# Optimization experiments

Measured on AMD Instinct MI355X. Metric: run time of the kernel, lower is better.

The kernel has to match this reference:

```python
import jax, jax.numpy as jnp
import numpy as np

D_MODEL = 1024
NUM_HEADS = 16
HEAD_DIM = D_MODEL // NUM_HEADS
FF_HIDDEN = 2 * D_MODEL
EPS = 1e-5


def _layernorm(x, g, b):
    mu = jnp.mean(x, axis=-1, keepdims=True)
    var = jnp.var(x, axis=-1, keepdims=True)
    return (x - mu) * jax.lax.rsqrt(var + EPS) * g + b


def setup_inputs() -> dict:
    key = jax.random.key(0)
    ks = jax.random.split(key, 12)
    s = lambda fan_in: 1.0 / np.sqrt(fan_in)
    return {
        "x": jax.random.normal(ks[0], (4, 2048, D_MODEL), dtype=jnp.float32),
        "qkv_w": jax.random.uniform(ks[1], (D_MODEL, 3 * D_MODEL), minval=-s(D_MODEL), maxval=s(D_MODEL)),
        "qkv_b": jax.random.uniform(ks[2], (3 * D_MODEL,), minval=-s(D_MODEL), maxval=s(D_MODEL)),
        "out_w": jax.random.uniform(ks[3], (D_MODEL, D_MODEL), minval=-s(D_MODEL), maxval=s(D_MODEL)),
        "out_b": jax.random.uniform(ks[4], (D_MODEL,), minval=-s(D_MODEL), maxval=s(D_MODEL)),
        "ff1_w": jax.random.uniform(ks[5], (D_MODEL, FF_HIDDEN), minval=-s(D_MODEL), maxval=s(D_MODEL)),
        "ff1_b": jax.random.uniform(ks[6], (FF_HIDDEN,), minval=-s(D_MODEL), maxval=s(D_MODEL)),
        "ff2_w": jax.random.uniform(ks[7], (FF_HIDDEN, D_MODEL), minval=-s(FF_HIDDEN), maxval=s(FF_HIDDEN)),
        "ff2_b": jax.random.uniform(ks[8], (D_MODEL,), minval=-s(FF_HIDDEN), maxval=s(FF_HIDDEN)),
        "ln1_g": jnp.ones((D_MODEL,), jnp.float32),
        "ln1_b": jnp.zeros((D_MODEL,), jnp.float32),
        "ln2_g": jnp.ones((D_MODEL,), jnp.float32),
        "ln2_b": jnp.zeros((D_MODEL,), jnp.float32),
    }


def reference(x, qkv_w, qkv_b, out_w, out_b, ff1_w, ff1_b, ff2_w, ff2_b, ln1_g, ln1_b, ln2_g, ln2_b):
    B, L, _ = x.shape
    scale = HEAD_DIM ** -0.5
    # pre-norm attention
    h = _layernorm(x, ln1_g, ln1_b)
    qkv = h @ qkv_w + qkv_b  # [B,L,3D]
    q, k, v = jnp.split(qkv, 3, axis=-1)
    reshape = lambda t: t.reshape(B, L, NUM_HEADS, HEAD_DIM).transpose(0, 2, 1, 3)  # [B,H,L,Dh]
    q, k, v = reshape(q), reshape(k), reshape(v)
    attn = jnp.einsum('bhqd,bhkd->bhqk', q, k) * scale  # [B,H,L,L]
    attn = jax.nn.softmax(attn, axis=-1)
    ctx = jnp.einsum('bhqk,bhkd->bhqd', attn, v)
    ctx = ctx.transpose(0, 2, 1, 3).reshape(B, L, D_MODEL)
    attended = ctx @ out_w + out_b
    x = x + attended
    # pre-norm FFN with exact GELU (torch default)
    h2 = _layernorm(x, ln2_g, ln2_b)
    ff = jax.nn.gelu(h2 @ ff1_w + ff1_b, approximate=False) @ ff2_w + ff2_b
    return x + ff
```

## Files before the change

kernel.cpp:

```cpp
#include <hip/hip_runtime.h>

#define AS1 __attribute__((address_space(1)))
#define AS3 __attribute__((address_space(3)))

typedef unsigned short u16;
typedef __bf16 bf16x8 __attribute__((ext_vector_type(8)));
typedef float floatx4 __attribute__((ext_vector_type(4)));
typedef float floatx16 __attribute__((ext_vector_type(16)));
typedef u16 u16x8 __attribute__((ext_vector_type(8)));
typedef u16 u16x4 __attribute__((ext_vector_type(4)));
typedef unsigned uintx4 __attribute__((ext_vector_type(4)));

__device__ __forceinline__ float bf2f(u16 u) { return __uint_as_float(((unsigned)u) << 16); }
__device__ __forceinline__ u16 f2bf(float f) {
    unsigned u = __float_as_uint(f);
    u += 0x7FFFu + ((u >> 16) & 1u);
    return (u16)(u >> 16);
}
__device__ __forceinline__ unsigned packbf2(float f0, float f1) {
    return __builtin_amdgcn_perm(__float_as_uint(f1), __float_as_uint(f0), 0x07060302u);
}
__device__ __forceinline__ float fexp2(float x) {
#if __has_builtin(__builtin_amdgcn_exp2f)
    return __builtin_amdgcn_exp2f(x);
#else
    float r;
    asm("v_exp_f32 %0, %1" : "=v"(r) : "v"(x));
    return r;
#endif
}
__device__ __forceinline__ void gl_lds16(const u16* g, u16* l) {
    __builtin_amdgcn_global_load_lds((const AS1 void*)g, (AS3 void*)l, 16, 0, 0);
}

__global__ __launch_bounds__(256) void transpose_all(const float* __restrict__ w0, u16* __restrict__ o0,
                                                     const float* __restrict__ w1, u16* __restrict__ o1,
                                                     const float* __restrict__ w2, u16* __restrict__ o2,
                                                     const float* __restrict__ w3, u16* __restrict__ o3) {
    __shared__ u16 t[32][33];
    int blk = blockIdx.x;
    const float* in;
    u16* out;
    int R, C, bx, by;
    if (blk < 3072) {
        in = w0; out = o0; R = 1024; C = 3072; bx = blk % 96; by = blk / 96;
    } else if (blk < 4096) {
        blk -= 3072; in = w1; out = o1; R = 1024; C = 1024; bx = blk % 32; by = blk / 32;
    } else if (blk < 6144) {
        blk -= 4096; in = w2; out = o2; R = 1024; C = 2048; bx = blk % 64; by = blk / 64;
    } else {
        blk -= 6144; in = w3; out = o3; R = 2048; C = 1024; bx = blk % 32; by = blk / 32;
    }
    const int c0 = bx * 32, r0 = by * 32;
    const int tx = threadIdx.x, ty = threadIdx.y;
#pragma unroll
    for (int i = 0; i < 4; i++)
        t[ty + i * 8][tx] = f2bf(in[(size_t)(r0 + ty + i * 8) * C + c0 + tx]);
    __syncthreads();
#pragma unroll
    for (int i = 0; i < 4; i++) out[(size_t)(c0 + ty + i * 8) * R + r0 + tx] = t[tx][ty + i * 8];
}

__global__ __launch_bounds__(256) void ln_k(const float* __restrict__ x, const float* __restrict__ g,
                                            const float* __restrict__ b, u16* __restrict__ out) {
    const int row = blockIdx.x, tid = threadIdx.x;
    const float4 xv = *(const float4*)(x + (size_t)row * 1024 + tid * 4);
    float f[4] = {xv.x, xv.y, xv.z, xv.w};
    float s1 = 0.f, s2 = 0.f;
#pragma unroll
    for (int e = 0; e < 4; e++) {
        s1 += f[e];
        s2 += f[e] * f[e];
    }
#pragma unroll
    for (int off = 32; off >= 1; off >>= 1) {
        s1 += __shfl_down(s1, off);
        s2 += __shfl_down(s2, off);
    }
    __shared__ float w1[4], w2[4];
    const int wave = tid >> 6, lane = tid & 63;
    if (lane == 0) { w1[wave] = s1; w2[wave] = s2; }
    __syncthreads();
    s1 = w1[0] + w1[1] + w1[2] + w1[3];
    s2 = w2[0] + w2[1] + w2[2] + w2[3];
    const float mu = s1 * (1.0f / 1024.0f);
    const float var = s2 * (1.0f / 1024.0f) - mu * mu;
    const float rs = rsqrtf(var + 1e-5f);
    const float4 gv = *(const float4*)(g + tid * 4);
    const float4 bv = *(const float4*)(b + tid * 4);
    const float gf[4] = {gv.x, gv.y, gv.z, gv.w}, bff[4] = {bv.x, bv.y, bv.z, bv.w};
    u16x4 o;
#pragma unroll
    for (int e = 0; e < 4; e++) o[e] = f2bf((f[e] - mu) * rs * gf[e] + bff[e]);
    *(u16x4*)(out + (size_t)row * 1024 + tid * 4) = o;
}

template <int GELU, int RESID, int F32OUT, int KSWZ>
__global__ __launch_bounds__(256, 4) void gemm_bt(const u16* __restrict__ A, const u16* __restrict__ Bt,
                                                  const float* __restrict__ bias,
                                                  const float* __restrict__ resid, void* __restrict__ Cv,
                                                  int M, int N, int K, int lda) {
    __shared__ u16 Al[2][128 * 32];
    __shared__ u16 Bl[2][128 * 32];
    const int tid = threadIdx.x;
    const int wave = tid >> 6, lane = tid & 63;
    const int g16 = lane >> 4, l16 = lane & 15;
    const int m0 = blockIdx.y * 128, n0 = blockIdx.x * 128;
    const int wm = (wave >> 1) * 64, wn = (wave & 1) * 64;
    const int csw = (l16 >> 1) & 3;

    floatx4 acc[4][4] = {};

    const int scs = ((lane & 3) ^ ((lane >> 3) & 3)) * 8;
    const u16* Ag = A + (size_t)(m0 + (lane >> 2)) * lda + scs;
    const u16* Bg = Bt + (size_t)(n0 + (lane >> 2)) * K + scs;

    auto stage = [&](int buf, int k0) {
#pragma unroll
        for (int i = 0; i < 2; i++) {
            const int ro = 16 * (wave * 2 + i);
            gl_lds16(Ag + (size_t)ro * lda + k0, &Al[buf][(wave * 2 + i) * 512]);
            gl_lds16(Bg + (size_t)ro * K + k0, &Bl[buf][(wave * 2 + i) * 512]);
        }
    };

    stage(0, 0);
    __syncthreads();
    int buf = 0;
    for (int k0 = 0; k0 < K; k0 += 32) {
        if (k0 + 32 < K) stage(buf ^ 1, k0 + 32);
        bf16x8 af[4], bfr[4];
#pragma unroll
        for (int i = 0; i < 4; i++)
            af[i] = *(const bf16x8*)&Al[buf][(wm + i * 16 + l16) * 32 + ((g16 ^ csw) << 3)];
#pragma unroll
        for (int j = 0; j < 4; j++)
            bfr[j] = *(const bf16x8*)&Bl[buf][(wn + j * 16 + l16) * 32 + ((g16 ^ csw) << 3)];
#pragma unroll
        for (int i = 0; i < 4; i++)
#pragma unroll
            for (int j = 0; j < 4; j++)
                acc[i][j] = __builtin_amdgcn_mfma_f32_16x16x32_bf16(af[i], bfr[j], acc[i][j], 0, 0, 0);
        __syncthreads();
        buf ^= 1;
    }

    float bv[4];
#pragma unroll
    for (int j = 0; j < 4; j++) bv[j] = bias[n0 + wn + j * 16 + l16];
#pragma unroll
    for (int i = 0; i < 4; i++) {
#pragma unroll
        for (int r = 0; r < 4; r++) {
            const int gm = m0 + wm + i * 16 + g16 * 4 + r;
            const size_t ro = (size_t)gm * N;
#pragma unroll
            for (int j = 0; j < 4; j++) {
                int gn = n0 + wn + j * 16 + l16;
                float v = acc[i][j][r] + bv[j];
                if (GELU) v = 0.5f * v * (1.0f + erff(v * 0.70710678118654752f));
                if (RESID) v += resid[ro + gn];
                if (KSWZ && ((gn >> 10) == 1)) gn ^= (gm & 7) << 3;
                if (F32OUT)
                    ((float*)Cv)[ro + gn] = v;
                else
                    ((u16*)Cv)[ro + gn] = f2bf(v);
            }
        }
    }
}

__global__ __launch_bounds__(256) void attn_prep(const u16* __restrict__ qkv, u16* __restrict__ Vsw) {
    __shared__ u16 Tl[64][72];
    const int bh = blockIdx.y, b = bh >> 4, h = bh & 15;
    const int kt = blockIdx.x * 64;
    const int t = threadIdx.x;
    const size_t qbase = (size_t)b * 2048 * 3072;
    const int r = t >> 2, cpi = (t & 3) * 2;

    const u16* vrow = qkv + qbase + (size_t)(kt + r) * 3072 + 2048 + h * 64;
    *(u16x8*)&Tl[r][cpi * 8] = *(const u16x8*)(vrow + cpi * 8);
    *(u16x8*)&Tl[r][(cpi + 1) * 8] = *(const u16x8*)(vrow + (cpi + 1) * 8);
    __syncthreads();
    {
        const int d = r;
        u16* dst = Vsw + ((size_t)bh * 64 + d) * 2048 + kt;
#pragma unroll
        for (int i = 0; i < 2; i++) {
            const int cp = cpi + i;
            const int c = cp ^ (d & 7);
            u16x8 tmp;
#pragma unroll
            for (int e = 0; e < 8; e++) tmp[e] = Tl[c * 8 + e][d];
            *(u16x8*)(dst + cp * 8) = tmp;
        }
    }
}

__global__ __launch_bounds__(256, 4) void attn_k(u16* __restrict__ qkv, const u16* __restrict__ Vsw) {
    __shared__ u16 Kl[2][64 * 64];
    __shared__ u16 Vt[2][64 * 64];
    const int tid = threadIdx.x;
    const int w = tid >> 6, lane = tid & 63;
    const int l31 = lane & 31, half = lane >> 5, swz = lane & 7;
    const int bh = blockIdx.y, b = bh >> 4, h = bh & 15;
    const int q0 = blockIdx.x * 128 + w * 32;
    const size_t qbase = (size_t)b * 2048 * 3072;
    const size_t vbase = (size_t)bh * 64 * 2048;

    bf16x8 bq[4];
    {
        const u16* qp = qkv + qbase + (size_t)(q0 + l31) * 3072 + h * 64;
        const float sc = 0.125f * 1.44269504088896340736f;
#pragma unroll
        for (int kd = 0; kd < 4; kd++) {
            const u16x8 raw = *(const u16x8*)(qp + kd * 16 + half * 8);
            u16 tmp[8];
#pragma unroll
            for (int e = 0; e < 8; e++) tmp[e] = f2bf(bf2f(raw[e]) * sc);
            bq[kd] = *(const bf16x8*)tmp;
        }
    }

    floatx16 accO[2] = {};
    float lsp[4] = {0.f, 0.f, 0.f, 0.f};

    auto stage = [&](int buf, int kt) {
#pragma unroll
        for (int i = 0; i < 2; i++) {
            const int rr = w * 16 + i * 8 + (lane >> 3);
            gl_lds16(qkv + qbase + (size_t)(kt + rr) * 3072 + 1024 + h * 64 + (lane & 7) * 8,
                     &Kl[buf][(w * 16 + i * 8) * 64]);
            gl_lds16(Vsw + vbase + (size_t)rr * 2048 + kt + (lane & 7) * 8,
                     &Vt[buf][(w * 16 + i * 8) * 64]);
        }
    };

    auto qk = [&](int bufi, floatx16* S) {
        floatx16 t[2] = {};
#pragma unroll
        for (int kb = 0; kb < 2; kb++)
#pragma unroll
            for (int kd = 0; kd < 4; kd++) {
                const bf16x8 ak =
                    *(const bf16x8*)&Kl[bufi][(kb * 32 + l31) * 64 + ((kd * 2 + half) ^ swz) * 8];
                t[kb] = __builtin_amdgcn_mfma_f32_32x32x16_bf16(ak, bq[kd], t[kb], 0, 0, 0);
            }
        S[0] = t[0];
        S[1] = t[1];
    };

    auto fused_sm_pv = [&](int bufi, const floatx16* S) {
#pragma unroll
        for (int kb = 0; kb < 2; kb++)
#pragma unroll
            for (int kp = 0; kp < 2; kp++) {
                float E[8];
#pragma unroll
                for (int j = 0; j < 8; j++) {
                    E[j] = fexp2(S[kb][8 * kp + j]);
                    lsp[j & 3] += E[j];
                }
                unsigned x0 = packbf2(E[0], E[1]);
                unsigned x1 = packbf2(E[2], E[3]);
                unsigned y0 = packbf2(E[4], E[5]);
                unsigned y1 = packbf2(E[6], E[7]);
                asm volatile("v_permlane32_swap_b32 %0, %1" : "+v"(x0), "+v"(y0));
                asm volatile("v_permlane32_swap_b32 %0, %1" : "+v"(x1), "+v"(y1));
                uintx4 f;
                f[0] = x0; f[1] = x1; f[2] = y0; f[3] = y1;
                const bf16x8 bp = __builtin_bit_cast(bf16x8, f);
                const int kd = kb * 2 + kp;
#pragma unroll
                for (int db = 0; db < 2; db++) {
                    const bf16x8 av =
                        *(const bf16x8*)&Vt[bufi][(db * 32 + l31) * 64 + ((kd * 2 + half) ^ swz) * 8];
                    accO[db] = __builtin_amdgcn_mfma_f32_32x32x16_bf16(av, bp, accO[db], 0, 0, 0);
                }
            }
    };

    stage(0, 0);
    __syncthreads();
    stage(1, 64);
    floatx16 accS[2];
    qk(0, accS);

    int buf = 0;
    for (int kt = 0; kt < 2048 - 64; kt += 64) {
        fused_sm_pv(buf, accS);
        __syncthreads();
        if (kt + 128 < 2048) stage(buf, kt + 128);
        __builtin_amdgcn_s_setprio(1);
        qk(buf ^ 1, accS);
        __builtin_amdgcn_s_setprio(0);
        buf ^= 1;
    }
    fused_sm_pv(buf, accS);

    float lsum = (lsp[0] + lsp[1]) + (lsp[2] + lsp[3]);
    lsum += __shfl_xor(lsum, 32);
    const float rinv = 1.0f / lsum;
    u16* cw = qkv + qbase + (size_t)(q0 + l31) * 3072 + 2048 + h * 64;
#pragma unroll
    for (int db = 0; db < 2; db++)
#pragma unroll
        for (int rg = 0; rg < 4; rg++) {
            const int d0 = db * 32 + 8 * rg + 4 * half;
            u16x4 o;
#pragma unroll
            for (int rr2 = 0; rr2 < 4; rr2++) o[rr2] = f2bf(accO[db][rg * 4 + rr2] * rinv);
            *(u16x4*)(cw + d0) = o;
        }
}

extern "C" void kernel_launch(void* const* d_in, const int* in_sizes, int n_in, void* d_out,
                              int out_size, void* d_ws, size_t ws_size, hipStream_t stream) {
    const float* x = (const float*)d_in[0];
    const float* qkv_w = (const float*)d_in[1];
    const float* qkv_b = (const float*)d_in[2];
    const float* out_w = (const float*)d_in[3];
    const float* out_b = (const float*)d_in[4];
    const float* ff1_w = (const float*)d_in[5];
    const float* ff1_b = (const float*)d_in[6];
    const float* ff2_w = (const float*)d_in[7];
    const float* ff2_b = (const float*)d_in[8];
    const float* ln1_g = (const float*)d_in[9];
    const float* ln1_b = (const float*)d_in[10];
    const float* ln2_g = (const float*)d_in[11];
    const float* ln2_b = (const float*)d_in[12];
    float* out = (float*)d_out;

    char* ws = (char*)d_ws;
    u16* qkvT = (u16*)(ws);
    u16* outT = (u16*)(ws + 6291456);
    u16* ff1T = (u16*)(ws + 8388608);
    u16* ff2T = (u16*)(ws + 12582912);
    u16* hbuf = (u16*)(ws + 16777216);
    u16* big  = (u16*)(ws + 33554432);

    transpose_all<<<8192, dim3(32, 8), 0, stream>>>(qkv_w, qkvT, out_w, outT, ff1_w, ff1T, ff2_w, ff2T);

    ln_k<<<8192, 256, 0, stream>>>(x, ln1_g, ln1_b, hbuf);
    gemm_bt<0, 0, 0, 1><<<dim3(24, 64), 256, 0, stream>>>(hbuf, qkvT, qkv_b, nullptr, big, 8192, 3072, 1024, 1024);
    attn_prep<<<dim3(32, 64), 256, 0, stream>>>(big, hbuf);
    attn_k<<<dim3(16, 64), 256, 0, stream>>>(big, hbuf);
    gemm_bt<0, 1, 1, 0><<<dim3(8, 64), 256, 0, stream>>>(big + 2048, outT, out_b, x, out, 8192, 1024, 1024, 3072);
    ln_k<<<8192, 256, 0, stream>>>(out, ln2_g, ln2_b, hbuf);
    gemm_bt<1, 0, 0, 0><<<dim3(16, 64), 256, 0, stream>>>(hbuf, ff1T, ff1_b, nullptr, big, 8192, 2048, 1024, 1024);
    gemm_bt<0, 1, 1, 0><<<dim3(8, 64), 256, 0, stream>>>(big, ff2T, ff2_b, out, out, 8192, 1024, 2048, 2048);
}
```

Baseline: 444.3 us.

## Triple-buffer K/V tiles in attention and overlap next QK with current PV

The attention kernel moves from double to triple buffering of K and V tiles in shared memory, with explicit vmcnt waits and raw barriers in place of __syncthreads. The loop is reordered so the QK^T product for the next tile is issued before the softmax/PV work of the current tile, and the score registers ping-pong between two sets. The aim is to hide global-to-LDS load latency and interleave MFMA chains from independent tiles. In exchange it uses more LDS, lowers the occupancy hint from 4 to 3 blocks, and raises register pressure.

```diff
diff --git a/kernel.cpp b/kernel.cpp
--- a/kernel.cpp
+++ b/kernel.cpp
@@ -197,9 +197,9 @@
     }
 }
 
-__global__ __launch_bounds__(256, 4) void attn_k(u16* __restrict__ qkv, const u16* __restrict__ Vsw) {
-    __shared__ u16 Kl[2][64 * 64];
-    __shared__ u16 Vt[2][64 * 64];
+__global__ __launch_bounds__(256, 3) void attn_k(u16* __restrict__ qkv, const u16* __restrict__ Vsw) {
+    __shared__ u16 Kl[3 * 64 * 64];
+    __shared__ u16 Vt[3 * 64 * 64];
     const int tid = threadIdx.x;
     const int w = tid >> 6, lane = tid & 63;
     const int l31 = lane & 31, half = lane >> 5, swz = lane & 7;
@@ -230,9 +230,9 @@
         for (int i = 0; i < 2; i++) {
             const int rr = w * 16 + i * 8 + (lane >> 3);
             gl_lds16(qkv + qbase + (size_t)(kt + rr) * 3072 + 1024 + h * 64 + (lane & 7) * 8,
-                     &Kl[buf][(w * 16 + i * 8) * 64]);
+                     &Kl[buf * 4096 + (w * 16 + i * 8) * 64]);
             gl_lds16(Vsw + vbase + (size_t)rr * 2048 + kt + (lane & 7) * 8,
-                     &Vt[buf][(w * 16 + i * 8) * 64]);
+                     &Vt[buf * 4096 + (w * 16 + i * 8) * 64]);
         }
     };
 
@@ -243,7 +243,7 @@
 #pragma unroll
             for (int kd = 0; kd < 4; kd++) {
                 const bf16x8 ak =
-                    *(const bf16x8*)&Kl[bufi][(kb * 32 + l31) * 64 + ((kd * 2 + half) ^ swz) * 8];
+                    *(const bf16x8*)&Kl[bufi * 4096 + (kb * 32 + l31) * 64 + ((kd * 2 + half) ^ swz) * 8];
                 t[kb] = __builtin_amdgcn_mfma_f32_32x32x16_bf16(ak, bq[kd], t[kb], 0, 0, 0);
             }
         S[0] = t[0];
@@ -274,29 +274,47 @@
 #pragma unroll
                 for (int db = 0; db < 2; db++) {
                     const bf16x8 av =
-                        *(const bf16x8*)&Vt[bufi][(db * 32 + l31) * 64 + ((kd * 2 + half) ^ swz) * 8];
+                        *(const bf16x8*)&Vt[bufi * 4096 + (db * 32 + l31) * 64 + ((kd * 2 + half) ^ swz) * 8];
                     accO[db] = __builtin_amdgcn_mfma_f32_32x32x16_bf16(av, bp, accO[db], 0, 0, 0);
                 }
             }
     };
 
+    auto iter = [&](int kt, int bc, int bn, int bs, floatx16* Sin, floatx16* Sout, bool do_stage) {
+        asm volatile("" ::: "memory");
+        __builtin_amdgcn_s_barrier();
+        asm volatile("" ::: "memory");
+        if (do_stage) {
+            stage(bs, kt + 128);
+            asm volatile("s_waitcnt vmcnt(4)" ::: "memory");
+        } else {
+            asm volatile("s_waitcnt vmcnt(0)" ::: "memory");
+        }
+        asm volatile("" ::: "memory");
+        __builtin_amdgcn_s_barrier();
+        asm volatile("" ::: "memory");
+        qk(bn, Sout);
+        fused_sm_pv(bc, Sin);
+    };
+
     stage(0, 0);
-    __syncthreads();
     stage(1, 64);
-    floatx16 accS[2];
-    qk(0, accS);
-
-    int buf = 0;
-    for (int kt = 0; kt < 2048 - 64; kt += 64) {
-        fused_sm_pv(buf, accS);
-        __syncthreads();
-        if (kt + 128 < 2048) stage(buf, kt + 128);
-        __builtin_amdgcn_s_setprio(1);
-        qk(buf ^ 1, accS);
-        __builtin_amdgcn_s_setprio(0);
-        buf ^= 1;
-    }
-    fused_sm_pv(buf, accS);
+    asm volatile("s_waitcnt vmcnt(4)" ::: "memory");
+    asm volatile("" ::: "memory");
+    __builtin_amdgcn_s_barrier();
+    asm volatile("" ::: "memory");
+
+    floatx16 sA[2], sB[2];
+    qk(0, sA);
+
+    int b0 = 0, b1 = 1, b2 = 2;
+    for (int kt = 0; kt < 30 * 64; kt += 128) {
+        iter(kt, b0, b1, b2, sA, sB, true);
+        iter(kt + 64, b1, b2, b0, sB, sA, true);
+        const int tmp = b0; b0 = b2; b2 = b1; b1 = tmp;
+    }
+    iter(30 * 64, b0, b1, b2, sA, sB, false);
+    fused_sm_pv(b1, sB);
 
     float lsum = (lsp[0] + lsp[1]) + (lsp[2] + lsp[3]);
     lsum += __shfl_xor(lsum, 32);
```

Measured after the change: 488.5 us. +9.9%, slower.
